# Optimization experiments

Hardware: AMD Instinct MI355X
Metric: run time of the kernel (lower is better)

## Reference

```python
import jax, jax.numpy as jnp
import numpy as np

N, C = 4194304, 10
EPS = 1e-10
FOCAL_EPS = 1e-8
TEMP, THETA = 0.01, 0.1
NUM_TH = 21


def setup_inputs() -> dict:
    key = jax.random.key(0)
    k1, k2 = jax.random.split(key)
    logits = jax.random.normal(k1, (N, C), dtype=jnp.float32)
    probs = jax.nn.softmax(logits, axis=1)
    labels = jax.random.randint(k2, (N,), 0, C)
    y = jax.nn.one_hot(labels, C, dtype=jnp.float32)
    return {"probs": probs, "y": y}


def _soft_T(e):
    # sigmoid( (1/temp) * log( e*(1-theta) / clamp((1-e)*theta, eps) ) )
    num = e * (1.0 - THETA)
    den = jnp.maximum((1.0 - e) * THETA, EPS)
    frac = jnp.maximum(num / den, EPS)
    return jax.nn.sigmoid(jnp.log(frac) / TEMP)


def reference(probs, y):
    entmax = jnp.log(jnp.asarray(C, dtype=probs.dtype))
    predictions = jnp.argmax(probs, axis=1)             # [N]
    labels = jnp.argmax(y)                              # scalar (flattened argmax, as in torch code)

    # predictive uncertainty (type=0): entropy of probs per-sample
    unc = -jnp.sum(probs * jnp.log(jnp.maximum(probs, EPS)), axis=1)  # [N]

    th_list = jnp.linspace(0.0, 1.0, NUM_TH, dtype=probs.dtype)       # [21]
    umin, umax = jnp.min(unc), jnp.max(unc)
    unc_th = umin + th_list * (umax - umin)                           # [21]

    s = _soft_T(unc / entmax)                                         # [N]
    t = jnp.tanh(unc)                                                 # [N]
    w_cert = (1.0 - s) * (1.0 - t)   # weight when counted as 'certain'
    w_unc = s * t                    # weight when counted as 'uncertain'

    acc = (predictions == labels).astype(probs.dtype)                 # [N]
    inacc = 1.0 - acc

    le = (unc[None, :] <= unc_th[:, None]).astype(probs.dtype)        # [21, N]
    gt = 1.0 - le

    # one parallel masked-reduction pass over all 21 thresholds
    n_ac = le @ (acc * w_cert)
    n_au = gt @ (acc * w_unc)
    n_ic = le @ (inacc * w_cert)
    n_iu = gt @ (inacc * w_unc)

    avu = (n_ac + n_iu) / (n_ac + n_au + n_ic + n_iu + EPS)           # [21]

    # trapezoid rule over increasing th_list (direction = +1)
    dx = jnp.diff(th_list)
    auc_avu = jnp.sum((avu[1:] + avu[:-1]) * 0.5 * dx)

    # FocalLoss(gamma=1)
    logp = jnp.log(jnp.maximum(probs, FOCAL_EPS))
    ce_per = -jnp.sum(y * logp, axis=1)
    focal_per = -jnp.sum(y * logp * (1.0 - probs), axis=1)
    focal_loss = jnp.mean(focal_per)
    ce_loss = jnp.mean(ce_per)

    beta = 1.0
    savu_loss = -beta * jnp.log(jnp.maximum(auc_avu, EPS)) + focal_loss
    return (savu_loss, ce_loss)
```

## Files before the change

### kernel.cpp

```cpp
#include <hip/hip_runtime.h>

#define C 10
#define CHUNK_ROWS 128
#define CHUNK_FLOATS 1280
#define CHUNK_F4 320

__device__ __forceinline__ float waveSum(float v) {
#pragma unroll
  for (int o = 32; o > 0; o >>= 1) v += __shfl_down(v, o, 64);
  return v;
}
__device__ __forceinline__ float waveMin(float v) {
#pragma unroll
  for (int o = 32; o > 0; o >>= 1) v = fminf(v, __shfl_down(v, o, 64));
  return v;
}
__device__ __forceinline__ float waveMax(float v) {
#pragma unroll
  for (int o = 32; o > 0; o >>= 1) v = fmaxf(v, __shfl_down(v, o, 64));
  return v;
}
__device__ __forceinline__ unsigned waveMaxU(unsigned v) {
#pragma unroll
  for (int o = 32; o > 0; o >>= 1) {
    unsigned w = (unsigned)__shfl_down((int)v, o, 64);
    v = v > w ? v : w;
  }
  return v;
}

__global__ __launch_bounds__(128, 4) void pass1(
    const float4* __restrict__ probs4, const float4* __restrict__ y4,
    float2* __restrict__ us2,
    unsigned* __restrict__ uminInvSlots, unsigned* __restrict__ umaxSlots,
    float* __restrict__ ceSlots, float* __restrict__ focalSlots,
    int nchunks) {
  __shared__ float lds[2 * 2 * CHUNK_FLOATS];
  const int widx = threadIdx.x >> 6, lane = threadIdx.x & 63;
  float4* const bufP = (float4*)(lds + widx * (2 * CHUNK_FLOATS));
  float4* const bufS = bufP + CHUNK_F4;

  const int gw = blockIdx.x * 2 + widx;
  const int NW = gridDim.x * 2;

  int label0 = 0;
  {
    const float* yf = (const float*)y4;
    float m = yf[0];
#pragma unroll
    for (int c = 1; c < C; ++c) {
      float v = yf[c];
      if (v > m) { m = v; label0 = c; }
    }
  }

  float4 P[5], Y[5];
  auto issue = [&](int c) {
    const float4* gp = probs4 + (size_t)c * CHUNK_F4 + lane;
    const float4* gy = y4 + (size_t)c * CHUNK_F4 + lane;
#pragma unroll
    for (int q = 0; q < 5; ++q) { P[q] = gp[q * 64]; Y[q] = gy[q * 64]; }
  };

  float ceA = 0.f, foA = 0.f;
  float mnA = __uint_as_float(0x7f800000u), mxA = 0.f;

  if (gw < nchunks) issue(gw);
  for (int c = gw; c < nchunks; c += NW) {
#pragma unroll
    for (int q = 0; q < 5; ++q) {
      float4 pv = P[q], yv = Y[q];
      float lpx = __logf(fmaxf(pv.x, 1e-10f));
      float lpy = __logf(fmaxf(pv.y, 1e-10f));
      float lpz = __logf(fmaxf(pv.z, 1e-10f));
      float lpw = __logf(fmaxf(pv.w, 1e-10f));
      float4 sv = make_float4(pv.x * lpx, pv.y * lpy, pv.z * lpz, pv.w * lpw);
      float tx = yv.x * fmaxf(lpx, -18.420681f);
      float ty = yv.y * fmaxf(lpy, -18.420681f);
      float tz = yv.z * fmaxf(lpz, -18.420681f);
      float tw = yv.w * fmaxf(lpw, -18.420681f);
      ceA -= tx + ty + tz + tw;
      foA -= tx * (1.f - pv.x) + ty * (1.f - pv.y) + tz * (1.f - pv.z) +
             tw * (1.f - pv.w);
      bufP[q * 64 + lane] = pv;
      bufS[q * 64 + lane] = sv;
    }

    if (c + NW < nchunks) issue(c + NW);

    float R[20], S[20];
#pragma unroll
    for (int q = 0; q < 5; ++q) {
      float4 v = bufP[lane * 5 + q];
      R[4 * q] = v.x; R[4 * q + 1] = v.y; R[4 * q + 2] = v.z; R[4 * q + 3] = v.w;
      float4 w = bufS[lane * 5 + q];
      S[4 * q] = w.x; S[4 * q + 1] = w.y; S[4 * q + 2] = w.z; S[4 * q + 3] = w.w;
    }
    int am0 = 0, am1 = 0;
    float m0 = R[0], m1 = R[10];
#pragma unroll
    for (int cc = 1; cc < C; ++cc) {
      if (R[cc] > m0) { m0 = R[cc]; am0 = cc; }
      if (R[10 + cc] > m1) { m1 = R[10 + cc]; am1 = cc; }
    }
    float u0 = -(((S[0] + S[1]) + (S[2] + S[3])) + ((S[4] + S[5]) + (S[6] + S[7])) +
                 (S[8] + S[9]));
    float u1 = -(((S[10] + S[11]) + (S[12] + S[13])) +
                 ((S[14] + S[15]) + (S[16] + S[17])) + (S[18] + S[19]));
    mnA = fminf(mnA, fminf(u0, u1));
    mxA = fmaxf(mxA, fmaxf(u0, u1));

    unsigned s0 = __float_as_uint(u0) | ((am0 == label0) ? 0u : 0x80000000u);
    unsigned s1 = __float_as_uint(u1) | ((am1 == label0) ? 0u : 0x80000000u);
    us2[(size_t)c * 64 + lane] = make_float2(__uint_as_float(s0), __uint_as_float(s1));
  }

  float ce = waveSum(ceA), fo = waveSum(foA);
  float mn = waveMin(mnA), mx = waveMax(mxA);
  if (lane == 0) {
    int slot = gw & 63;
    atomicAdd(&ceSlots[slot], ce);
    atomicAdd(&focalSlots[slot], fo);
    atomicMax(&uminInvSlots[slot], ~__float_as_uint(mn));
    atomicMax(&umaxSlots[slot], __float_as_uint(mx));
  }
}

__global__ __launch_bounds__(256, 4) void pass2(
    const float4* __restrict__ us4, int n4,
    const unsigned* __restrict__ uminInvSlots, const unsigned* __restrict__ umaxSlots,
    float* __restrict__ ghist) {
  __shared__ float hist[88 * 64];
  __shared__ float smm[2];
  const int tid = threadIdx.x, lane = tid & 63;
  for (int i = tid; i < 88 * 64; i += 256) hist[i] = 0.f;
  if (tid < 64) {
    unsigned mnInv = waveMaxU(uminInvSlots[tid]);
    unsigned mxb = waveMaxU(umaxSlots[tid]);
    if (tid == 0) { smm[0] = __uint_as_float(~mnInv); smm[1] = __uint_as_float(mxb); }
  }
  __syncthreads();
  const float umin = smm[0], delta = smm[1] - smm[0];
  float th[21];
#pragma unroll
  for (int k = 0; k < 21; ++k) th[k] = fmaf(0.05f * (float)k, delta, umin);

  const int stride = gridDim.x * 256;
  for (int i = blockIdx.x * 256 + tid; i < n4; i += stride) {
    float4 v = us4[i];
    float vv[4] = {v.x, v.y, v.z, v.w};
#pragma unroll
    for (int q = 0; q < 4; ++q) {
      unsigned b = __float_as_uint(vv[q]);
      int rb = (b >> 31) ? 44 : 0;
      float u = __uint_as_float(b & 0x7fffffffu);
      float e = u * 0.4342944819f;
      float lnum = __logf(e * 0.9f);
      float lden = __logf(fmaxf((1.f - e) * 0.1f, 1e-10f));
      float x = fmaxf(lnum - lden, -23.0258509f) * 100.f;
      float s = __builtin_amdgcn_rcpf(1.f + __expf(-x));
      float t = 1.f - 2.f * __builtin_amdgcn_rcpf(__expf(2.f * u) + 1.f);
      float wc = (1.f - s) * (1.f - t), wu = s * t;
      int j = 0;
#pragma unroll
      for (int k = 0; k < 21; ++k) j += (u > th[k]) ? 1 : 0;
      atomicAdd(&hist[(rb + j) * 64 + lane], wc);
      atomicAdd(&hist[(rb + 22 + j) * 64 + lane], wu);
    }
  }
  __syncthreads();
#pragma unroll
  for (int st = 32; st >= 1; st >>= 1) {
    for (int idx = tid; idx < 88 * st; idx += 256) {
      int r = idx / st, c = idx - r * st;
      hist[r * 64 + c] += hist[r * 64 + c + st];
    }
    __syncthreads();
  }
  int slot = blockIdx.x & 63;
  for (int r = tid; r < 88; r += 256)
    atomicAdd(&ghist[slot * 88 + r], hist[r * 64]);
}

__global__ __launch_bounds__(256) void pass3(
    const float* __restrict__ ghist,
    const float* __restrict__ ceSlots, const float* __restrict__ focalSlots,
    float* __restrict__ out, float invN) {
  __shared__ float hr[88];
  __shared__ float scf[2];
  int tid = threadIdx.x;
  if (tid < 88) {
    float s = 0.f;
    for (int q = 0; q < 64; ++q) s += ghist[q * 88 + tid];
    hr[tid] = s;
  }
  if (tid >= 128 && tid < 192) {
    int l = tid - 128;
    float ce = waveSum(ceSlots[l]);
    float fo = waveSum(focalSlots[l]);
    if (l == 0) { scf[0] = ce; scf[1] = fo; }
  }
  __syncthreads();
  if (tid == 0) {
    float H0[22], H1[22], H2[22], H3[22];
    float totAU = 0.f, totIU = 0.f;
    for (int j = 0; j < 22; ++j) {
      H0[j] = hr[j]; H1[j] = hr[22 + j]; H2[j] = hr[44 + j]; H3[j] = hr[66 + j];
      totAU += H1[j]; totIU += H3[j];
    }
    float n_ac = 0.f, n_ic = 0.f, n_au = totAU, n_iu = totIU;
    float auc = 0.f, prev = 0.f;
    for (int k = 0; k < 21; ++k) {
      n_ac += H0[k]; n_ic += H2[k];
      n_au -= H1[k]; n_iu -= H3[k];
      float avu = (n_ac + n_iu) / (n_ac + n_au + n_ic + n_iu + 1e-10f);
      if (k > 0) auc += (avu + prev) * 0.5f * 0.05f;
      prev = avu;
    }
    out[0] = -logf(fmaxf(auc, 1e-10f)) + scf[1] * invN;
    out[1] = scf[0] * invN;
  }
}

extern "C" void kernel_launch(void* const* d_in, const int* in_sizes, int n_in,
                              void* d_out, int out_size, void* d_ws, size_t ws_size,
                              hipStream_t stream) {
  const float* probs = (const float*)d_in[0];
  const float* y = (const float*)d_in[1];
  float* out = (float*)d_out;
  const int N = in_sizes[0] / C;

  float* wsf = (float*)d_ws;
  unsigned* uminInvSlots = (unsigned*)wsf;
  unsigned* umaxSlots = (unsigned*)(wsf + 64);
  float* ceSlots = wsf + 128;
  float* focalSlots = wsf + 192;
  float* ghist = wsf + 256;
  float* us = wsf + 5888;

  hipMemsetAsync(d_ws, 0, 5888 * sizeof(float), stream);

  const int nchunks = N / CHUNK_ROWS;
  pass1<<<2048, 128, 0, stream>>>((const float4*)probs, (const float4*)y,
                                  (float2*)us, uminInvSlots, umaxSlots,
                                  ceSlots, focalSlots, nchunks);
  pass2<<<1024, 256, 0, stream>>>((const float4*)us, N / 4, uminInvSlots, umaxSlots,
                                  ghist);
  pass3<<<1, 256, 0, stream>>>(ghist, ceSlots, focalSlots, out, 1.0f / (float)N);
}
```

Baseline: 385.7 us.

## Fuse three passes into one cooperative kernel keeping uncertainties in registers

```diff
diff --git a/kernel.cpp b/kernel.cpp
--- a/kernel.cpp
+++ b/kernel.cpp
@@ -1,4 +1,7 @@
 #include <hip/hip_runtime.h>
+#include <hip/hip_cooperative_groups.h>
+
+namespace cg = cooperative_groups;
 
 #define C 10
 #define CHUNK_ROWS 128
@@ -27,6 +30,190 @@
     v = v > w ? v : w;
   }
   return v;
+}
+
+#define GLD16(gp, lp)                                             \
+  __builtin_amdgcn_global_load_lds(                               \
+      (__attribute__((address_space(1))) void*)(gp),              \
+      (__attribute__((address_space(3))) void*)(lp), 16, 0, 0)
+
+__device__ __forceinline__ void binSample(unsigned b, const float* th,
+                                          int& rb, int& j, float& wc, float& wu) {
+  rb = (b >> 31) ? 44 : 0;
+  float u = __uint_as_float(b & 0x7fffffffu);
+  float e = u * 0.4342944819f;
+  float lnum = __logf(e * 0.9f);
+  float lden = __logf(fmaxf((1.f - e) * 0.1f, 1e-10f));
+  float x = fmaxf(lnum - lden, -23.0258509f) * 100.f;
+  float s = __builtin_amdgcn_rcpf(1.f + __expf(-x));
+  float t = 1.f - 2.f * __builtin_amdgcn_rcpf(__expf(2.f * u) + 1.f);
+  wc = (1.f - s) * (1.f - t);
+  wu = s * t;
+  j = 0;
+#pragma unroll
+  for (int k = 0; k < 21; ++k) j += (u > th[k]) ? 1 : 0;
+}
+
+__global__ __launch_bounds__(256, 4) void mega(
+    const float* __restrict__ probs, const float* __restrict__ y,
+    unsigned* __restrict__ uminInvSlots, unsigned* __restrict__ umaxSlots,
+    float* __restrict__ ceSlots, float* __restrict__ focalSlots,
+    float* __restrict__ ghist, float* __restrict__ out, float invN) {
+  __shared__ float lds[88 * 64];
+  __shared__ float smm[2];
+  const int tid = threadIdx.x, lane = tid & 63, widx = tid >> 6;
+  cg::grid_group grid = cg::this_grid();
+
+  int label0 = 0;
+  {
+    float m = y[0];
+#pragma unroll
+    for (int c = 1; c < C; ++c) {
+      float v = y[c];
+      if (v > m) { m = v; label0 = c; }
+    }
+  }
+
+  float au[16];
+  float ceA = 0.f, foA = 0.f;
+  float mnA = __uint_as_float(0x7f800000u), mxA = 0.f;
+  const size_t blockBase = (size_t)blockIdx.x * (8 * 5120);
+  const float2* b2 = (const float2*)lds;
+
+#pragma unroll 1
+  for (int t = 0; t < 8; ++t) {
+    const size_t base = blockBase + (size_t)t * 5120;
+#pragma unroll
+    for (int k = 0; k < 5; ++k) {
+      int idx = k * 256 + tid;
+      GLD16(probs + base + (size_t)idx * 4, lds + idx * 4);
+    }
+    __syncthreads();
+    float P0[10], P1[10];
+#pragma unroll
+    for (int j = 0; j < 5; ++j) {
+      float2 v = b2[tid * 5 + j];
+      P0[2 * j] = v.x; P0[2 * j + 1] = v.y;
+      float2 w = b2[(tid + 256) * 5 + j];
+      P1[2 * j] = w.x; P1[2 * j + 1] = w.y;
+    }
+    __syncthreads();
+#pragma unroll
+    for (int k = 0; k < 5; ++k) {
+      int idx = k * 256 + tid;
+      GLD16(y + base + (size_t)idx * 4, lds + idx * 4);
+    }
+    int am0 = 0, am1 = 0;
+    float m0 = P0[0], m1 = P1[0];
+#pragma unroll
+    for (int cc = 1; cc < C; ++cc) {
+      if (P0[cc] > m0) { m0 = P0[cc]; am0 = cc; }
+      if (P1[cc] > m1) { m1 = P1[cc]; am1 = cc; }
+    }
+    float u0 = 0.f, u1 = 0.f;
+#pragma unroll
+    for (int cc = 0; cc < C; ++cc) {
+      u0 -= P0[cc] * __logf(fmaxf(P0[cc], 1e-10f));
+      u1 -= P1[cc] * __logf(fmaxf(P1[cc], 1e-10f));
+    }
+    mnA = fminf(mnA, fminf(u0, u1));
+    mxA = fmaxf(mxA, fmaxf(u0, u1));
+    au[2 * t] = __uint_as_float(__float_as_uint(u0) |
+                                ((am0 == label0) ? 0u : 0x80000000u));
+    au[2 * t + 1] = __uint_as_float(__float_as_uint(u1) |
+                                    ((am1 == label0) ? 0u : 0x80000000u));
+    __syncthreads();
+    float pl0 = 0.f, pl1 = 0.f;
+#pragma unroll
+    for (int j = 0; j < 5; ++j) {
+      float2 v = b2[tid * 5 + j];
+      pl0 = fmaf(v.x, P0[2 * j], pl0); pl0 = fmaf(v.y, P0[2 * j + 1], pl0);
+      float2 w = b2[(tid + 256) * 5 + j];
+      pl1 = fmaf(w.x, P1[2 * j], pl1); pl1 = fmaf(w.y, P1[2 * j + 1], pl1);
+    }
+    float ce0 = -__logf(fmaxf(pl0, 1e-8f)), ce1 = -__logf(fmaxf(pl1, 1e-8f));
+    ceA += ce0 + ce1;
+    foA += ce0 * (1.f - pl0) + ce1 * (1.f - pl1);
+    __syncthreads();
+  }
+
+  {
+    float ce = waveSum(ceA), fo = waveSum(foA);
+    float mn = waveMin(mnA), mx = waveMax(mxA);
+    if (lane == 0) {
+      int slot = (blockIdx.x * 4 + widx) & 63;
+      atomicAdd(&ceSlots[slot], ce);
+      atomicAdd(&focalSlots[slot], fo);
+      atomicMax(&uminInvSlots[slot], ~__float_as_uint(mn));
+      atomicMax(&umaxSlots[slot], __float_as_uint(mx));
+    }
+  }
+  grid.sync();
+
+  if (tid < 64) {
+    unsigned mnInv = waveMaxU(uminInvSlots[tid]);
+    unsigned mxb = waveMaxU(umaxSlots[tid]);
+    if (tid == 0) { smm[0] = __uint_as_float(~mnInv); smm[1] = __uint_as_float(mxb); }
+  }
+  for (int i = tid; i < 88 * 64; i += 256) lds[i] = 0.f;
+  __syncthreads();
+  {
+    const float umin = smm[0], delta = smm[1] - smm[0];
+    float th[21];
+#pragma unroll
+    for (int k = 0; k < 21; ++k) th[k] = fmaf(0.05f * (float)k, delta, umin);
+#pragma unroll
+    for (int i = 0; i < 16; ++i) {
+      int rb, j; float wc, wu;
+      binSample(__float_as_uint(au[i]), th, rb, j, wc, wu);
+      atomicAdd(&lds[(rb + j) * 64 + lane], wc);
+      atomicAdd(&lds[(rb + 22 + j) * 64 + lane], wu);
+    }
+  }
+  __syncthreads();
+#pragma unroll
+  for (int st = 32; st >= 1; st >>= 1) {
+    for (int idx = tid; idx < 88 * st; idx += 256) {
+      int r = idx / st, c = idx - r * st;
+      lds[r * 64 + c] += lds[r * 64 + c + st];
+    }
+    __syncthreads();
+  }
+  {
+    int slot = blockIdx.x & 63;
+    for (int r = tid; r < 88; r += 256) atomicAdd(&ghist[slot * 88 + r], lds[r * 64]);
+  }
+  grid.sync();
+
+  if (blockIdx.x == 0) {
+    if (tid < 88) {
+      float s = 0.f;
+      for (int q = 0; q < 64; ++q) s += ghist[q * 88 + tid];
+      lds[tid] = s;
+    }
+    if (tid >= 128 && tid < 192) {
+      int l = tid - 128;
+      float ce = waveSum(ceSlots[l]);
+      float fo = waveSum(focalSlots[l]);
+      if (l == 0) { smm[0] = ce; smm[1] = fo; }
+    }
+    __syncthreads();
+    if (tid == 0) {
+      float totAU = 0.f, totIU = 0.f;
+      for (int j = 0; j < 22; ++j) { totAU += lds[22 + j]; totIU += lds[66 + j]; }
+      float n_ac = 0.f, n_ic = 0.f, n_au = totAU, n_iu = totIU;
+      float auc = 0.f, prev = 0.f;
+      for (int k = 0; k < 21; ++k) {
+        n_ac += lds[k]; n_ic += lds[44 + k];
+        n_au -= lds[22 + k]; n_iu -= lds[66 + k];
+        float avu = (n_ac + n_iu) / (n_ac + n_au + n_ic + n_iu + 1e-10f);
+        if (k > 0) auc += (avu + prev) * 0.5f * 0.05f;
+        prev = avu;
+      }
+      out[0] = -logf(fmaxf(auc, 1e-10f)) + smm[1] * invN;
+      out[1] = smm[0] * invN;
+    }
+  }
 }
 
 __global__ __launch_bounds__(128, 4) void pass1(
@@ -39,10 +226,8 @@
   const int widx = threadIdx.x >> 6, lane = threadIdx.x & 63;
   float4* const bufP = (float4*)(lds + widx * (2 * CHUNK_FLOATS));
   float4* const bufS = bufP + CHUNK_F4;
-
   const int gw = blockIdx.x * 2 + widx;
   const int NW = gridDim.x * 2;
-
   int label0 = 0;
   {
     const float* yf = (const float*)y4;
@@ -53,7 +238,6 @@
       if (v > m) { m = v; label0 = c; }
     }
   }
-
   float4 P[5], Y[5];
   auto issue = [&](int c) {
     const float4* gp = probs4 + (size_t)c * CHUNK_F4 + lane;
@@ -61,10 +245,8 @@
 #pragma unroll
     for (int q = 0; q < 5; ++q) { P[q] = gp[q * 64]; Y[q] = gy[q * 64]; }
   };
-
   float ceA = 0.f, foA = 0.f;
   float mnA = __uint_as_float(0x7f800000u), mxA = 0.f;
-
   if (gw < nchunks) issue(gw);
   for (int c = gw; c < nchunks; c += NW) {
 #pragma unroll
@@ -85,9 +267,7 @@
       bufP[q * 64 + lane] = pv;
       bufS[q * 64 + lane] = sv;
     }
-
     if (c + NW < nchunks) issue(c + NW);
-
     float R[20], S[20];
 #pragma unroll
     for (int q = 0; q < 5; ++q) {
@@ -109,12 +289,10 @@
                  ((S[14] + S[15]) + (S[16] + S[17])) + (S[18] + S[19]));
     mnA = fminf(mnA, fminf(u0, u1));
     mxA = fmaxf(mxA, fmaxf(u0, u1));
-
     unsigned s0 = __float_as_uint(u0) | ((am0 == label0) ? 0u : 0x80000000u);
     unsigned s1 = __float_as_uint(u1) | ((am1 == label0) ? 0u : 0x80000000u);
     us2[(size_t)c * 64 + lane] = make_float2(__uint_as_float(s0), __uint_as_float(s1));
   }
-
   float ce = waveSum(ceA), fo = waveSum(foA);
   float mn = waveMin(mnA), mx = waveMax(mxA);
   if (lane == 0) {
@@ -144,26 +322,14 @@
   float th[21];
 #pragma unroll
   for (int k = 0; k < 21; ++k) th[k] = fmaf(0.05f * (float)k, delta, umin);
-
   const int stride = gridDim.x * 256;
   for (int i = blockIdx.x * 256 + tid; i < n4; i += stride) {
     float4 v = us4[i];
     float vv[4] = {v.x, v.y, v.z, v.w};
 #pragma unroll
     for (int q = 0; q < 4; ++q) {
-      unsigned b = __float_as_uint(vv[q]);
-      int rb = (b >> 31) ? 44 : 0;
-      float u = __uint_as_float(b & 0x7fffffffu);
-      float e = u * 0.4342944819f;
-      float lnum = __logf(e * 0.9f);
-      float lden = __logf(fmaxf((1.f - e) * 0.1f, 1e-10f));
-      float x = fmaxf(lnum - lden, -23.0258509f) * 100.f;
-      float s = __builtin_amdgcn_rcpf(1.f + __expf(-x));
-      float t = 1.f - 2.f * __builtin_amdgcn_rcpf(__expf(2.f * u) + 1.f);
-      float wc = (1.f - s) * (1.f - t), wu = s * t;
-      int j = 0;
-#pragma unroll
-      for (int k = 0; k < 21; ++k) j += (u > th[k]) ? 1 : 0;
+      int rb, j; float wc, wu;
+      binSample(__float_as_uint(vv[q]), th, rb, j, wc, wu);
       atomicAdd(&hist[(rb + j) * 64 + lane], wc);
       atomicAdd(&hist[(rb + 22 + j) * 64 + lane], wu);
     }
@@ -178,8 +344,7 @@
     __syncthreads();
   }
   int slot = blockIdx.x & 63;
-  for (int r = tid; r < 88; r += 256)
-    atomicAdd(&ghist[slot * 88 + r], hist[r * 64]);
+  for (int r = tid; r < 88; r += 256) atomicAdd(&ghist[slot * 88 + r], hist[r * 64]);
 }
 
 __global__ __launch_bounds__(256) void pass3(
@@ -202,17 +367,13 @@
   }
   __syncthreads();
   if (tid == 0) {
-    float H0[22], H1[22], H2[22], H3[22];
     float totAU = 0.f, totIU = 0.f;
-    for (int j = 0; j < 22; ++j) {
-      H0[j] = hr[j]; H1[j] = hr[22 + j]; H2[j] = hr[44 + j]; H3[j] = hr[66 + j];
-      totAU += H1[j]; totIU += H3[j];
-    }
+    for (int j = 0; j < 22; ++j) { totAU += hr[22 + j]; totIU += hr[66 + j]; }
     float n_ac = 0.f, n_ic = 0.f, n_au = totAU, n_iu = totIU;
     float auc = 0.f, prev = 0.f;
     for (int k = 0; k < 21; ++k) {
-      n_ac += H0[k]; n_ic += H2[k];
-      n_au -= H1[k]; n_iu -= H3[k];
+      n_ac += hr[k]; n_ic += hr[44 + k];
+      n_au -= hr[22 + k]; n_iu -= hr[66 + k];
       float avu = (n_ac + n_iu) / (n_ac + n_au + n_ic + n_iu + 1e-10f);
       if (k > 0) auc += (avu + prev) * 0.5f * 0.05f;
       prev = avu;
@@ -229,6 +390,7 @@
   const float* y = (const float*)d_in[1];
   float* out = (float*)d_out;
   const int N = in_sizes[0] / C;
+  float invN = 1.0f / (float)N;
 
   float* wsf = (float*)d_ws;
   unsigned* uminInvSlots = (unsigned*)wsf;
@@ -240,11 +402,18 @@
 
   hipMemsetAsync(d_ws, 0, 5888 * sizeof(float), stream);
 
-  const int nchunks = N / CHUNK_ROWS;
-  pass1<<<2048, 128, 0, stream>>>((const float4*)probs, (const float4*)y,
-                                  (float2*)us, uminInvSlots, umaxSlots,
-                                  ceSlots, focalSlots, nchunks);
-  pass2<<<1024, 256, 0, stream>>>((const float4*)us, N / 4, uminInvSlots, umaxSlots,
-                                  ghist);
-  pass3<<<1, 256, 0, stream>>>(ghist, ceSlots, focalSlots, out, 1.0f / (float)N);
-}
+  void* args[] = {(void*)&probs, (void*)&y, (void*)&uminInvSlots,
+                  (void*)&umaxSlots, (void*)&ceSlots, (void*)&focalSlots,
+                  (void*)&ghist, (void*)&out, (void*)&invN};
+  hipError_t e = hipLaunchCooperativeKernel((const void*)mega, dim3(1024),
+                                            dim3(256), args, 0, stream);
+  if (e != hipSuccess) {
+    const int nchunks = N / CHUNK_ROWS;
+    pass1<<<2048, 128, 0, stream>>>((const float4*)probs, (const float4*)y,
+                                    (float2*)us, uminInvSlots, umaxSlots,
+                                    ceSlots, focalSlots, nchunks);
+    pass2<<<1024, 256, 0, stream>>>((const float4*)us, N / 4, uminInvSlots,
+                                    umaxSlots, ghist);
+    pass3<<<1, 256, 0, stream>>>(ghist, ceSlots, focalSlots, out, invN);
+  }
+}
```

New measurement: 616.2 us. 59.8% more time.
